# Performance work log

Measured on AMD Instinct MI355X. Metric: run time of the kernel, lower is better.

## Reference

```python
import jax, jax.numpy as jnp
from jax import lax
import numpy as np
import math

D_MODEL = 1024
D_STATE = 16
DT_RANK = 64  # ceil(1024/16)


def setup_inputs() -> dict:
    key = jax.random.key(0)
    ks = jax.random.split(key, 8)
    B, L = 2, 2048
    x = jax.random.normal(ks[0], (B, L, D_MODEL), dtype=jnp.float32)
    A_log = jnp.full((D_MODEL, D_STATE), math.log(0.5), dtype=jnp.float32)
    x_proj_w = jax.random.normal(ks[1], (DT_RANK + 2 * D_STATE, D_MODEL), dtype=jnp.float32) * (D_MODEL ** -0.5)
    dt_init_std = DT_RANK ** -0.5
    dt_proj_w = jax.random.uniform(ks[2], (D_MODEL, DT_RANK), minval=-dt_init_std, maxval=dt_init_std, dtype=jnp.float32)
    # dt bias init: softplus-inverse of dt sampled log-uniform in [2*dt_min, 2*dt_max] (trend)
    dt = jnp.exp(jax.random.uniform(ks[3], (D_MODEL,), dtype=jnp.float32) * (math.log(0.2) - math.log(0.002)) + math.log(0.002))
    dt = jnp.clip(dt, 1e-4)
    dt_proj_b = dt + jnp.log(-jnp.expm1(-dt))
    D_param = jnp.ones((D_MODEL,), dtype=jnp.float32)
    trend_emphasis = jnp.full((D_MODEL,), 0.1, dtype=jnp.float32)
    return {
        "x": x, "A_log": A_log, "x_proj_w": x_proj_w,
        "dt_proj_w": dt_proj_w, "dt_proj_b": dt_proj_b,
        "D_param": D_param, "trend_emphasis": trend_emphasis,
    }


def _selective_scan(u, delta, A, Bp, Cp, D_param):
    # u, delta: [B,L,D]; A: [D,N]; Bp, Cp: [B,L,N]; D_param: [D]
    deltaA = jnp.exp(jnp.einsum('bld,dn->bldn', delta, A))       # [B,L,D,N]
    deltaBu = jnp.einsum('bld,bln->bldn', delta * u, Bp)          # [B,L,D,N]
    Bsz, L, Dm, N = deltaA.shape

    def step(h, inp):
        dA, dBu, c = inp          # dA,dBu: [B,D,N]; c: [B,N]
        h = dA * h + dBu
        y = jnp.einsum('bdn,bn->bd', h, c)
        return h, y

    h0 = jnp.zeros((Bsz, Dm, N), dtype=u.dtype)
    xs = (jnp.moveaxis(deltaA, 1, 0), jnp.moveaxis(deltaBu, 1, 0), jnp.moveaxis(Cp, 1, 0))
    _, ys = lax.scan(step, h0, xs)            # ys: [L,B,D]
    y = jnp.moveaxis(ys, 0, 1)                # [B,L,D]
    return y + u * D_param


def reference(x, A_log, x_proj_w, dt_proj_w, dt_proj_b, D_param, trend_emphasis):
    # trend component: channel-wise emphasis gate (dropout in eval mode = identity)
    x = x * jax.nn.sigmoid(trend_emphasis)
    xz = x @ x_proj_w.T                                  # [B,L,dt_rank+2N]
    delta_part = xz[..., :DT_RANK]
    Bp = xz[..., DT_RANK:DT_RANK + D_STATE]              # [B,L,N]
    Cp = xz[..., DT_RANK + D_STATE:]                     # [B,L,N]
    delta = jax.nn.softplus(delta_part @ dt_proj_w.T + dt_proj_b)  # [B,L,D]
    A = -jnp.exp(A_log.astype(jnp.float32))
    return _selective_scan(x, delta, A, Bp, Cp, D_param.astype(jnp.float32))
```

## Files before the change

### kernel.cpp

```cpp
#include <hip/hip_runtime.h>
#include <math.h>


#define LOG2E 1.44269504088896340736f
typedef float v2f __attribute__((ext_vector_type(2)));

__device__ __forceinline__ float fexp2(float v){
#if defined(__has_builtin)
#if __has_builtin(__builtin_amdgcn_exp2f)
  return __builtin_amdgcn_exp2f(v);
#else
  return exp2f(v);
#endif
#else
  return exp2f(v);
#endif
}

__device__ __forceinline__ float fsoftplus(float v){
  return fmaxf(v, 0.f) + __logf(1.f + __expf(-fabsf(v)));
}

__global__ __launch_bounds__(256) void k_prep(const float* __restrict__ xpw,
                                              const float* __restrict__ dtw,
                                              const float* __restrict__ alog,
                                              const float* __restrict__ te,
                                              float* __restrict__ w2T,
                                              float* __restrict__ dtwT,
                                              float* __restrict__ A2,
                                              float* __restrict__ sg){
  __shared__ float sm[32 * 33];
  const int bid = blockIdx.x, t = threadIdx.x;
  const int lane = t & 31, srow = t >> 5;
  if (bid < 96){
    const int kt = bid / 3, ct = bid - kt * 3;
#pragma unroll
    for (int r = 0; r < 4; r++){
      const int cr = srow * 4 + r;
      sm[cr * 33 + lane] = xpw[(size_t)(ct * 32 + cr) * 1024 + kt * 32 + lane];
    }
    __syncthreads();
#pragma unroll
    for (int r = 0; r < 4; r++){
      const int kr = srow * 4 + r;
      const int kg = kt * 32 + kr;
      const float s = 1.f / (1.f + __expf(-te[kg]));
      w2T[(size_t)kg * 96 + ct * 32 + lane] = sm[lane * 33 + kr] * s;
    }
  } else if (bid < 160){
    const int idx = bid - 96, dti = idx >> 1, kt2 = idx & 1;
#pragma unroll
    for (int r = 0; r < 4; r++){
      const int cr = srow * 4 + r;
      sm[cr * 33 + lane] = dtw[(size_t)(dti * 32 + cr) * 64 + kt2 * 32 + lane];
    }
    __syncthreads();
#pragma unroll
    for (int r = 0; r < 4; r++){
      const int kr = srow * 4 + r;
      dtwT[(size_t)(kt2 * 32 + kr) * 1024 + dti * 32 + lane] = sm[lane * 33 + kr];
    }
  } else if (bid < 176){
    const int j = (bid - 160) * 1024 + t;
#pragma unroll
    for (int i = 0; i < 4; i++)
      A2[j + i * 256] = -__expf(alog[j + i * 256]) * LOG2E;
  } else {
#pragma unroll
    for (int i = 0; i < 4; i++){
      const int m = i * 256 + t;
      sg[m] = 1.f / (1.f + __expf(-te[m]));
    }
  }
}

__global__ __launch_bounds__(256) void k_xz(const float* __restrict__ x,
                                            const float* __restrict__ w2T,
                                            float* __restrict__ xzp){
  __shared__ float xT[32 * 257];
  const int t = threadIdx.x;
  const int row0 = blockIdx.x * 256;
  const int c0 = blockIdx.y * 32;
  const int kbase = blockIdx.z * 128;
  v2f acc[16];
#pragma unroll
  for (int c = 0; c < 16; c++) acc[c] = (v2f){0.f, 0.f};
  const int kq = t & 7, rsub = t >> 3;
  for (int kt = 0; kt < 4; ++kt){
    const int k0 = kbase + kt * 32;
    __syncthreads();
#pragma unroll
    for (int p = 0; p < 8; p++){
      const int r = p * 32 + rsub;
      const float4 v = *reinterpret_cast<const float4*>(&x[(size_t)(row0 + r) * 1024 + k0 + kq * 4]);
      xT[(kq * 4 + 0) * 257 + r] = v.x;
      xT[(kq * 4 + 1) * 257 + r] = v.y;
      xT[(kq * 4 + 2) * 257 + r] = v.z;
      xT[(kq * 4 + 3) * 257 + r] = v.w;
    }
    __syncthreads();
#pragma unroll 4
    for (int kk = 0; kk < 32; ++kk){
      const float xv = xT[kk * 257 + t];
      const v2f xv2 = {xv, xv};
      const v2f* wr = reinterpret_cast<const v2f*>(&w2T[(size_t)(k0 + kk) * 96 + c0]);
#pragma unroll
      for (int c = 0; c < 16; c++) acc[c] = acc[c] + xv2 * wr[c];
    }
  }
  float4* o = reinterpret_cast<float4*>(xzp + ((size_t)blockIdx.z * 4096 + row0 + t) * 96 + c0);
  const float4* av = reinterpret_cast<const float4*>(acc);
#pragma unroll
  for (int q = 0; q < 8; q++) o[q] = av[q];
}

__global__ __launch_bounds__(256) void k_reduce(const float4* __restrict__ p,
                                                float4* __restrict__ xz){
  const int i = blockIdx.x * 256 + threadIdx.x;
  float4 r = p[i];
#pragma unroll
  for (int s = 1; s < 8; s++){
    const float4 a = p[(size_t)s * 98304 + i];
    r.x += a.x; r.y += a.y; r.z += a.z; r.w += a.w;
  }
  xz[i] = r;
}

__global__ __launch_bounds__(256) void k_delta(const float* __restrict__ xz,
                                               const float* __restrict__ dtwT,
                                               const float* __restrict__ dtb,
                                               float* __restrict__ del){
  const int t = threadIdx.x;
  const int r0 = blockIdx.x * 16;
  const int d = blockIdx.y * 256 + t;
  v2f wv[32];
#pragma unroll
  for (int k2 = 0; k2 < 32; k2++){
    wv[k2].x = dtwT[(size_t)(2 * k2) * 1024 + d];
    wv[k2].y = dtwT[(size_t)(2 * k2 + 1) * 1024 + d];
  }
  const float dtbv = dtb[d];
  const float* xzb = xz + (size_t)r0 * 96;
#pragma unroll 4
  for (int li = 0; li < 16; ++li){
    v2f acc = {dtbv, 0.f};
    const v2f* dp = reinterpret_cast<const v2f*>(xzb + li * 96);
#pragma unroll
    for (int k2 = 0; k2 < 32; k2++) acc = acc + dp[k2] * wv[k2];
    del[(size_t)(r0 + li) * 1024 + d] = fsoftplus(acc.x + acc.y);
  }
}

__global__ __launch_bounds__(256) void k_scan1(const float* __restrict__ x,
                                               const float* __restrict__ del,
                                               const float* __restrict__ xz,
                                               const float* __restrict__ A2,
                                               const float* __restrict__ sg,
                                               float* __restrict__ S,
                                               float* __restrict__ P){
  const int t = threadIdx.x;
  const int chunk = blockIdx.x, dgrp = blockIdx.y, b = blockIdx.z;
  const int d = dgrp * 256 + t;
  const int l0 = chunk * 32;
  float a2[16];
  {
    const float4* ap = reinterpret_cast<const float4*>(A2 + (size_t)d * 16);
#pragma unroll
    for (int q = 0; q < 4; q++){
      const float4 v = ap[q];
      a2[q*4] = v.x; a2[q*4+1] = v.y; a2[q*4+2] = v.z; a2[q*4+3] = v.w;
    }
  }
  bool uni = true;
#pragma unroll
  for (int n = 1; n < 16; n++) uni = uni && (a2[n] == a2[0]);
  const float sgv = sg[d];
  const size_t xidx0 = (size_t)(b * 2048 + l0) * 1024 + d;
  const float* xzb = xz + (size_t)(b * 2048 + l0) * 96;
  const size_t base = ((size_t)((b * 64 + chunk) * 1024 + d)) * 16;
  if (uni){
    const float a2u = a2[0];
    v2f h2[8];
#pragma unroll
    for (int q = 0; q < 8; q++) h2[q] = (v2f){0.f, 0.f};
    float sumd = 0.f;
    for (int ph = 0; ph < 2; ++ph){
      const size_t xidx = xidx0 + (size_t)ph * 16 * 1024;
      float dl[16], du[16];
#pragma unroll
      for (int li = 0; li < 16; ++li){
        dl[li] = del[xidx + (size_t)li * 1024];
        du[li] = dl[li] * x[xidx + (size_t)li * 1024] * sgv;
      }
#pragma unroll 4
      for (int li = 0; li < 16; ++li){
        sumd += dl[li];
        const float tt = fexp2(dl[li] * a2u);
        const v2f tt2 = {tt, tt}, du2 = {du[li], du[li]};
        const v2f* brow = reinterpret_cast<const v2f*>(xzb + (ph * 16 + li) * 96 + 64);
#pragma unroll
        for (int q = 0; q < 8; q++) h2[q] = h2[q] * tt2 + brow[q] * du2;
      }
    }
    const float Ppu = fexp2(a2u * sumd);
    const float4* hv = reinterpret_cast<const float4*>(h2);
#pragma unroll
    for (int q = 0; q < 4; q++)
      *reinterpret_cast<float4*>(&S[base + q * 4]) = hv[q];
    const float4 pv = {Ppu, Ppu, Ppu, Ppu};
#pragma unroll
    for (int q = 0; q < 4; q++)
      *reinterpret_cast<float4*>(&P[base + q * 4]) = pv;
  } else {
    float h[16], Pp[16];
#pragma unroll
    for (int n = 0; n < 16; n++){ h[n] = 0.f; Pp[n] = 1.f; }
    for (int li = 0; li < 32; ++li){
      const float dv = del[xidx0 + (size_t)li * 1024];
      const float duv = dv * x[xidx0 + (size_t)li * 1024] * sgv;
      const float* brow = xzb + li * 96 + 64;
#pragma unroll
      for (int n = 0; n < 16; n++){
        const float tt = fexp2(dv * a2[n]);
        h[n] = fmaf(tt, h[n], duv * brow[n]);
        Pp[n] *= tt;
      }
    }
#pragma unroll
    for (int q = 0; q < 4; q++){
      float4 v; v.x = h[q*4]; v.y = h[q*4+1]; v.z = h[q*4+2]; v.w = h[q*4+3];
      *reinterpret_cast<float4*>(&S[base + q * 4]) = v;
      float4 u; u.x = Pp[q*4]; u.y = Pp[q*4+1]; u.z = Pp[q*4+2]; u.w = Pp[q*4+3];
      *reinterpret_cast<float4*>(&P[base + q * 4]) = u;
    }
  }
}

__global__ __launch_bounds__(256) void k_scan2(const float* __restrict__ S,
                                               const float* __restrict__ P,
                                               float* __restrict__ H){
  __shared__ float ls[256], lp[256];
  const int t = threadIdx.x;
  const int dn = t & 31, seg = t >> 5;
  const int n = dn & 15, dloc = dn >> 4;
  const int bid = blockIdx.x;
  const int b = bid >> 9, dpair = bid & 511;
  const int d = dpair * 2 + dloc;
  const size_t sbase = ((size_t)(b * 64) * 1024 + d) * 16 + n;
  float Sv[8], Pv[8];
  float s = 0.f, p = 1.f;
#pragma unroll
  for (int i = 0; i < 8; i++){
    const size_t idx = sbase + (size_t)(seg * 8 + i) * 16384;
    Sv[i] = S[idx]; Pv[i] = P[idx];
    s = fmaf(Pv[i], s, Sv[i]);
    p *= Pv[i];
  }
  ls[t] = s; lp[t] = p;
  __syncthreads();
  float h = 0.f;
  for (int j = 0; j < seg; j++)
    h = fmaf(lp[j * 32 + dn], h, ls[j * 32 + dn]);
#pragma unroll
  for (int i = 0; i < 8; i++){
    const size_t idx = sbase + (size_t)(seg * 8 + i) * 16384;
    H[idx] = h;
    h = fmaf(Pv[i], h, Sv[i]);
  }
}

__global__ __launch_bounds__(256) void k_scan3(const float* __restrict__ x,
                                               const float* __restrict__ del,
                                               const float* __restrict__ xz,
                                               const float* __restrict__ A2,
                                               const float* __restrict__ sg,
                                               const float* __restrict__ Dpar,
                                               const float* __restrict__ H,
                                               float* __restrict__ out){
  const int t = threadIdx.x;
  const int chunk = blockIdx.x, dgrp = blockIdx.y, b = blockIdx.z;
  const int d = dgrp * 256 + t;
  const int l0 = chunk * 32;
  float a2[16];
  {
    const float4* ap = reinterpret_cast<const float4*>(A2 + (size_t)d * 16);
#pragma unroll
    for (int q = 0; q < 4; q++){
      const float4 v = ap[q];
      a2[q*4] = v.x; a2[q*4+1] = v.y; a2[q*4+2] = v.z; a2[q*4+3] = v.w;
    }
  }
  bool uni = true;
#pragma unroll
  for (int n = 1; n < 16; n++) uni = uni && (a2[n] == a2[0]);
  const float sgv = sg[d], Dv = Dpar[d];
  const size_t xidx0 = (size_t)(b * 2048 + l0) * 1024 + d;
  const float* xzb = xz + (size_t)(b * 2048 + l0) * 96;
  const size_t hbase = ((size_t)((b * 64 + chunk) * 1024 + d)) * 16;
  if (uni){
    const float a2u = a2[0];
    v2f h2[8];
    {
      const float4* hp = reinterpret_cast<const float4*>(H + hbase);
      float4* hd = reinterpret_cast<float4*>(h2);
#pragma unroll
      for (int q = 0; q < 4; q++) hd[q] = hp[q];
    }
    for (int ph = 0; ph < 2; ++ph){
      const size_t xidx = xidx0 + (size_t)ph * 16 * 1024;
      float dl[16], xd[16];
#pragma unroll
      for (int li = 0; li < 16; ++li){
        dl[li] = del[xidx + (size_t)li * 1024];
        xd[li] = x[xidx + (size_t)li * 1024] * sgv;
      }
#pragma unroll 4
      for (int li = 0; li < 16; ++li){
        const float duv = dl[li] * xd[li];
        const float tt = fexp2(dl[li] * a2u);
        const v2f tt2 = {tt, tt}, du2 = {duv, duv};
        const v2f* brow = reinterpret_cast<const v2f*>(xzb + (ph * 16 + li) * 96 + 64);
        const v2f* crow = reinterpret_cast<const v2f*>(xzb + (ph * 16 + li) * 96 + 80);
        v2f yv = {0.f, 0.f};
#pragma unroll
        for (int q = 0; q < 8; q++){
          h2[q] = h2[q] * tt2 + brow[q] * du2;
          yv = yv + h2[q] * crow[q];
        }
        out[xidx + (size_t)li * 1024] = fmaf(xd[li], Dv, yv.x + yv.y);
      }
    }
  } else {
    float h[16];
    {
      const float4* hp = reinterpret_cast<const float4*>(H + hbase);
#pragma unroll
      for (int q = 0; q < 4; q++){
        const float4 v = hp[q];
        h[q*4] = v.x; h[q*4+1] = v.y; h[q*4+2] = v.z; h[q*4+3] = v.w;
      }
    }
    for (int li = 0; li < 32; ++li){
      const float dv = del[xidx0 + (size_t)li * 1024];
      const float xdv = x[xidx0 + (size_t)li * 1024] * sgv;
      const float duv = dv * xdv;
      const float* brow = xzb + li * 96 + 64;
      float y = 0.f;
#pragma unroll
      for (int n = 0; n < 16; n++){
        const float tt = fexp2(dv * a2[n]);
        h[n] = fmaf(tt, h[n], duv * brow[n]);
        y = fmaf(h[n], brow[16 + n], y);
      }
      out[xidx0 + (size_t)li * 1024] = fmaf(xdv, Dv, y);
    }
  }
}

extern "C" void kernel_launch(void* const* d_in, const int* in_sizes, int n_in,
                              void* d_out, int out_size, void* d_ws, size_t ws_size,
                              hipStream_t stream){
  const float* x    = (const float*)d_in[0];
  const float* Alog = (const float*)d_in[1];
  const float* xpw  = (const float*)d_in[2];
  const float* dtw  = (const float*)d_in[3];
  const float* dtb  = (const float*)d_in[4];
  const float* Dpar = (const float*)d_in[5];
  const float* te   = (const float*)d_in[6];
  float* out = (float*)d_out;
  char* ws = (char*)d_ws;

  float* w2T  = (float*)(ws);
  float* A2   = (float*)(ws + 393216);
  float* sg   = (float*)(ws + 458752);
  float* dtwT = (float*)(ws + 462848);
  float* xz   = (float*)(ws + 724992);
  float* del  = (float*)(ws + 2297856);
  float* xzp  = (float*)(ws + 19075072);
  float* S    = (float*)(ws + 31657984);
  float* P    = (float*)(ws + 40046592);
  float* Hst  = (float*)(ws + 48435200);

  hipLaunchKernelGGL(k_prep,   dim3(177),        dim3(256), 0, stream, xpw, dtw, Alog, te, w2T, dtwT, A2, sg);
  hipLaunchKernelGGL(k_xz,     dim3(16, 3, 8),   dim3(256), 0, stream, x, w2T, xzp);
  hipLaunchKernelGGL(k_reduce, dim3(384),        dim3(256), 0, stream, (const float4*)xzp, (float4*)xz);
  hipLaunchKernelGGL(k_delta,  dim3(256, 4),     dim3(256), 0, stream, xz, dtwT, dtb, del);
  hipLaunchKernelGGL(k_scan1,  dim3(64, 4, 2),   dim3(256), 0, stream, x, del, xz, A2, sg, S, P);
  hipLaunchKernelGGL(k_scan2,  dim3(1024),       dim3(256), 0, stream, S, P, Hst);
  hipLaunchKernelGGL(k_scan3,  dim3(64, 4, 2),   dim3(256), 0, stream, x, del, xz, A2, sg, Dpar, Hst, out);
}
```

Baseline: 161.3 us.

## Replace split-K partial buffer and reduce kernel with atomic accumulation; inline A/sigmoid prep

The split-K projection now accumulates its partial sums directly into the zeroed xz buffer with float atomicAdd, which removes the separate reduce kernel and the large partial-sum buffer round trip. A memset is added to clear xz before accumulation. A2 and the sigmoid gate are now computed inline in the scan kernels from A_log and trend_emphasis rather than precomputed in prep. Atomics make the summation order nondeterministic and add contention on the same rows from eight K-slices, and the inline exp calls add a little work to the scan kernels.

```diff
diff --git a/kernel.cpp b/kernel.cpp
--- a/kernel.cpp
+++ b/kernel.cpp
@@ -23,12 +23,9 @@
 
 __global__ __launch_bounds__(256) void k_prep(const float* __restrict__ xpw,
                                               const float* __restrict__ dtw,
-                                              const float* __restrict__ alog,
                                               const float* __restrict__ te,
                                               float* __restrict__ w2T,
-                                              float* __restrict__ dtwT,
-                                              float* __restrict__ A2,
-                                              float* __restrict__ sg){
+                                              float* __restrict__ dtwT){
   __shared__ float sm[32 * 33];
   const int bid = blockIdx.x, t = threadIdx.x;
   const int lane = t & 31, srow = t >> 5;
@@ -47,7 +44,7 @@
       const float s = 1.f / (1.f + __expf(-te[kg]));
       w2T[(size_t)kg * 96 + ct * 32 + lane] = sm[lane * 33 + kr] * s;
     }
-  } else if (bid < 160){
+  } else {
     const int idx = bid - 96, dti = idx >> 1, kt2 = idx & 1;
 #pragma unroll
     for (int r = 0; r < 4; r++){
@@ -60,23 +57,12 @@
       const int kr = srow * 4 + r;
       dtwT[(size_t)(kt2 * 32 + kr) * 1024 + dti * 32 + lane] = sm[lane * 33 + kr];
     }
-  } else if (bid < 176){
-    const int j = (bid - 160) * 1024 + t;
-#pragma unroll
-    for (int i = 0; i < 4; i++)
-      A2[j + i * 256] = -__expf(alog[j + i * 256]) * LOG2E;
-  } else {
-#pragma unroll
-    for (int i = 0; i < 4; i++){
-      const int m = i * 256 + t;
-      sg[m] = 1.f / (1.f + __expf(-te[m]));
-    }
   }
 }
 
 __global__ __launch_bounds__(256) void k_xz(const float* __restrict__ x,
                                             const float* __restrict__ w2T,
-                                            float* __restrict__ xzp){
+                                            float* __restrict__ xz){
   __shared__ float xT[32 * 257];
   const int t = threadIdx.x;
   const int row0 = blockIdx.x * 256;
@@ -108,22 +94,10 @@
       for (int c = 0; c < 16; c++) acc[c] = acc[c] + xv2 * wr[c];
     }
   }
-  float4* o = reinterpret_cast<float4*>(xzp + ((size_t)blockIdx.z * 4096 + row0 + t) * 96 + c0);
-  const float4* av = reinterpret_cast<const float4*>(acc);
-#pragma unroll
-  for (int q = 0; q < 8; q++) o[q] = av[q];
-}
-
-__global__ __launch_bounds__(256) void k_reduce(const float4* __restrict__ p,
-                                                float4* __restrict__ xz){
-  const int i = blockIdx.x * 256 + threadIdx.x;
-  float4 r = p[i];
-#pragma unroll
-  for (int s = 1; s < 8; s++){
-    const float4 a = p[(size_t)s * 98304 + i];
-    r.x += a.x; r.y += a.y; r.z += a.z; r.w += a.w;
-  }
-  xz[i] = r;
+  float* xzrow = xz + (size_t)(row0 + t) * 96 + c0;
+  const float* av = reinterpret_cast<const float*>(acc);
+#pragma unroll
+  for (int c = 0; c < 32; c++) atomicAdd(&xzrow[c], av[c]);
 }
 
 __global__ __launch_bounds__(256) void k_delta(const float* __restrict__ xz,
@@ -154,8 +128,8 @@
 __global__ __launch_bounds__(256) void k_scan1(const float* __restrict__ x,
                                                const float* __restrict__ del,
                                                const float* __restrict__ xz,
-                                               const float* __restrict__ A2,
-                                               const float* __restrict__ sg,
+                                               const float* __restrict__ alog,
+                                               const float* __restrict__ te,
                                                float* __restrict__ S,
                                                float* __restrict__ P){
   const int t = threadIdx.x;
@@ -164,17 +138,18 @@
   const int l0 = chunk * 32;
   float a2[16];
   {
-    const float4* ap = reinterpret_cast<const float4*>(A2 + (size_t)d * 16);
+    const float4* ap = reinterpret_cast<const float4*>(alog + (size_t)d * 16);
 #pragma unroll
     for (int q = 0; q < 4; q++){
       const float4 v = ap[q];
-      a2[q*4] = v.x; a2[q*4+1] = v.y; a2[q*4+2] = v.z; a2[q*4+3] = v.w;
+      a2[q*4+0] = -__expf(v.x) * LOG2E; a2[q*4+1] = -__expf(v.y) * LOG2E;
+      a2[q*4+2] = -__expf(v.z) * LOG2E; a2[q*4+3] = -__expf(v.w) * LOG2E;
     }
   }
   bool uni = true;
 #pragma unroll
   for (int n = 1; n < 16; n++) uni = uni && (a2[n] == a2[0]);
-  const float sgv = sg[d];
+  const float sgv = 1.f / (1.f + __expf(-te[d]));
   const size_t xidx0 = (size_t)(b * 2048 + l0) * 1024 + d;
   const float* xzb = xz + (size_t)(b * 2048 + l0) * 96;
   const size_t base = ((size_t)((b * 64 + chunk) * 1024 + d)) * 16;
@@ -272,8 +247,8 @@
 __global__ __launch_bounds__(256) void k_scan3(const float* __restrict__ x,
                                                const float* __restrict__ del,
                                                const float* __restrict__ xz,
-                                               const float* __restrict__ A2,
-                                               const float* __restrict__ sg,
+                                               const float* __restrict__ alog,
+                                               const float* __restrict__ te,
                                                const float* __restrict__ Dpar,
                                                const float* __restrict__ H,
                                                float* __restrict__ out){
@@ -283,17 +258,19 @@
   const int l0 = chunk * 32;
   float a2[16];
   {
-    const float4* ap = reinterpret_cast<const float4*>(A2 + (size_t)d * 16);
+    const float4* ap = reinterpret_cast<const float4*>(alog + (size_t)d * 16);
 #pragma unroll
     for (int q = 0; q < 4; q++){
       const float4 v = ap[q];
-      a2[q*4] = v.x; a2[q*4+1] = v.y; a2[q*4+2] = v.z; a2[q*4+3] = v.w;
+      a2[q*4+0] = -__expf(v.x) * LOG2E; a2[q*4+1] = -__expf(v.y) * LOG2E;
+      a2[q*4+2] = -__expf(v.z) * LOG2E; a2[q*4+3] = -__expf(v.w) * LOG2E;
     }
   }
   bool uni = true;
 #pragma unroll
   for (int n = 1; n < 16; n++) uni = uni && (a2[n] == a2[0]);
-  const float sgv = sg[d], Dv = Dpar[d];
+  const float sgv = 1.f / (1.f + __expf(-te[d]));
+  const float Dv = Dpar[d];
   const size_t xidx0 = (size_t)(b * 2048 + l0) * 1024 + d;
   const float* xzb = xz + (size_t)(b * 2048 + l0) * 96;
   const size_t hbase = ((size_t)((b * 64 + chunk) * 1024 + d)) * 16;
@@ -371,21 +348,18 @@
   char* ws = (char*)d_ws;
 
   float* w2T  = (float*)(ws);
-  float* A2   = (float*)(ws + 393216);
-  float* sg   = (float*)(ws + 458752);
-  float* dtwT = (float*)(ws + 462848);
-  float* xz   = (float*)(ws + 724992);
-  float* del  = (float*)(ws + 2297856);
-  float* xzp  = (float*)(ws + 19075072);
-  float* S    = (float*)(ws + 31657984);
-  float* P    = (float*)(ws + 40046592);
-  float* Hst  = (float*)(ws + 48435200);
-
-  hipLaunchKernelGGL(k_prep,   dim3(177),        dim3(256), 0, stream, xpw, dtw, Alog, te, w2T, dtwT, A2, sg);
-  hipLaunchKernelGGL(k_xz,     dim3(16, 3, 8),   dim3(256), 0, stream, x, w2T, xzp);
-  hipLaunchKernelGGL(k_reduce, dim3(384),        dim3(256), 0, stream, (const float4*)xzp, (float4*)xz);
-  hipLaunchKernelGGL(k_delta,  dim3(256, 4),     dim3(256), 0, stream, xz, dtwT, dtb, del);
-  hipLaunchKernelGGL(k_scan1,  dim3(64, 4, 2),   dim3(256), 0, stream, x, del, xz, A2, sg, S, P);
-  hipLaunchKernelGGL(k_scan2,  dim3(1024),       dim3(256), 0, stream, S, P, Hst);
-  hipLaunchKernelGGL(k_scan3,  dim3(64, 4, 2),   dim3(256), 0, stream, x, del, xz, A2, sg, Dpar, Hst, out);
-}
+  float* dtwT = (float*)(ws + 393216);
+  float* xz   = (float*)(ws + 655360);
+  float* del  = (float*)(ws + 2228224);
+  float* S    = (float*)(ws + 19005440);
+  float* P    = (float*)(ws + 27394048);
+  float* Hst  = (float*)(ws + 35782656);
+
+  hipMemsetAsync(xz, 0, 1572864, stream);
+  hipLaunchKernelGGL(k_prep,   dim3(160),       dim3(256), 0, stream, xpw, dtw, te, w2T, dtwT);
+  hipLaunchKernelGGL(k_xz,     dim3(16, 3, 8),  dim3(256), 0, stream, x, w2T, xz);
+  hipLaunchKernelGGL(k_delta,  dim3(256, 4),    dim3(256), 0, stream, xz, dtwT, dtb, del);
+  hipLaunchKernelGGL(k_scan1,  dim3(64, 4, 2),  dim3(256), 0, stream, x, del, xz, Alog, te, S, P);
+  hipLaunchKernelGGL(k_scan2,  dim3(1024),      dim3(256), 0, stream, S, P, Hst);
+  hipLaunchKernelGGL(k_scan3,  dim3(64, 4, 2),  dim3(256), 0, stream, x, del, xz, Alog, te, Dpar, Hst, out);
+}
```

Measured after the change: 316.2 us. +96.0%, slower.
